# Performance work log

Hardware: AMD Instinct MI355X
Metric: run time of the kernel (lower is better)

The kernel has to match this reference:

```python
import jax, jax.numpy as jnp
import numpy as np

H = 4  # hidden_size
L = 2  # num_layers


def _lstm_cell(x, h, c, Wih, Whh, bih, bhh):
    # PyTorch gate order: input, forget, cell(g), output
    gates = x @ Wih.T + h @ Whh.T + (bih + bhh)  # [B, 4H]
    i, f, g, o = jnp.split(gates, 4, axis=-1)
    i = jax.nn.sigmoid(i)
    f = jax.nn.sigmoid(f)
    g = jnp.tanh(g)
    o = jax.nn.sigmoid(o)
    c_new = f * c + i * g
    h_new = o * jnp.tanh(c_new)
    return h_new, c_new


def setup_inputs() -> dict:
    key = jax.random.key(0)
    ks = jax.random.split(key, 24)
    B, S, D, T = 32768, 256, 8, 12
    s = 1.0 / np.sqrt(H)  # PyTorch LSTM init scale

    def u(k, shape):
        return jax.random.uniform(k, shape, jnp.float32, -s, s)

    inp = {
        "src": jax.random.normal(ks[0], (B, S, D), jnp.float32),
        "trg": jax.random.normal(ks[1], (B, T, 1), jnp.float32),
        # encoder LSTM (input_dim=8 -> H, then H -> H)
        "enc_Wih0": u(ks[2], (4 * H, D)), "enc_Whh0": u(ks[3], (4 * H, H)),
        "enc_bih0": u(ks[4], (4 * H,)), "enc_bhh0": u(ks[5], (4 * H,)),
        "enc_Wih1": u(ks[6], (4 * H, H)), "enc_Whh1": u(ks[7], (4 * H, H)),
        "enc_bih1": u(ks[8], (4 * H,)), "enc_bhh1": u(ks[9], (4 * H,)),
        # decoder LSTM (input_dim=1 -> H, then H -> H)
        "dec_Wih0": u(ks[10], (4 * H, 1)), "dec_Whh0": u(ks[11], (4 * H, H)),
        "dec_bih0": u(ks[12], (4 * H,)), "dec_bhh0": u(ks[13], (4 * H,)),
        "dec_Wih1": u(ks[14], (4 * H, H)), "dec_Whh1": u(ks[15], (4 * H, H)),
        "dec_bih1": u(ks[16], (4 * H,)), "dec_bhh1": u(ks[17], (4 * H,)),
        # fc: hidden -> 1
        "fc_W": u(ks[18], (1, H)), "fc_b": u(ks[19], (1,)),
    }
    return inp


def reference(src, trg,
              enc_Wih0, enc_Whh0, enc_bih0, enc_bhh0,
              enc_Wih1, enc_Whh1, enc_bih1, enc_bhh1,
              dec_Wih0, dec_Whh0, dec_bih0, dec_bhh0,
              dec_Wih1, dec_Whh1, dec_bih1, dec_bhh1,
              fc_W, fc_b):
    B, T = src.shape[0], trg.shape[1]
    enc_layers = [(enc_Wih0, enc_Whh0, enc_bih0, enc_bhh0),
                  (enc_Wih1, enc_Whh1, enc_bih1, enc_bhh1)]
    dec_layers = [(dec_Wih0, dec_Whh0, dec_bih0, dec_bhh0),
                  (dec_Wih1, dec_Whh1, dec_bih1, dec_bhh1)]

    def multi_step(layers, h, c, x):
        new_h, new_c, inp = [], [], x
        for l, p in enumerate(layers):
            hl, cl = _lstm_cell(inp, h[l], c[l], *p)
            new_h.append(hl); new_c.append(cl); inp = hl
        return jnp.stack(new_h), jnp.stack(new_c), inp

    # ---- encoder: scan over src time steps ----
    h0 = jnp.zeros((L, B, H), src.dtype)
    c0 = jnp.zeros((L, B, H), src.dtype)

    def enc_step(carry, x_t):
        h, c = carry
        h, c, _ = multi_step(enc_layers, h, c, x_t)
        return (h, c), None

    (h, c), _ = jax.lax.scan(enc_step, (h0, c0), jnp.swapaxes(src, 0, 1))

    x0 = trg[:, 0, :]  # [B, 1]

    def dec_step(carry, _):
        h, c, x = carry
        h, c, top = multi_step(dec_layers, h, c, x)
        pred = top @ fc_W.T + fc_b  # [B, 1]
        return (h, c, pred), pred

    _, preds = jax.lax.scan(dec_step, (h, c, x0), None, length=T - 1)  # [T-1, B, 1]
    outputs = jnp.concatenate([x0[None], preds], axis=0)  # [T, B, 1]
    return jnp.swapaxes(outputs, 0, 1)  # [B, T, 1]
```

## Files before the change

kernel.cpp:

```cpp
#include <hip/hip_runtime.h>

namespace {

constexpr int Sn = 256;
constexpr int Tn = 12;
constexpr float L2E = 1.44269504088896340736f;

typedef float v2f __attribute__((ext_vector_type(2)));

__device__ __forceinline__ v2f pkfma(v2f a, v2f b, v2f c) {
  return __builtin_elementwise_fma(a, b, c);
}

__device__ __forceinline__ float rcp_(float x) { return __builtin_amdgcn_rcpf(x); }

#if __has_builtin(__builtin_amdgcn_exp2f)
__device__ __forceinline__ float exp2_(float x) { return __builtin_amdgcn_exp2f(x); }
#else
__device__ __forceinline__ float exp2_(float x) { return __expf(x * 0.69314718055994530942f); }
#endif

template <int CTRL>
__device__ __forceinline__ float qperm(float v) {
  return __int_as_float(
      __builtin_amdgcn_mov_dpp(__float_as_int(v), CTRL, 0xF, 0xF, true));
}
constexpr int DPP_XOR1 = 0xB1;
constexpr int DPP_XOR2 = 0x4E;
constexpr int DPP_XOR3 = 0x1B;
constexpr int DPP_BC0 = 0x00;

__device__ __forceinline__ float unit_update(v2f g01, v2f g23, float& c) {
  float ei = exp2_(g01.x);
  float ef = exp2_(g01.y);
  float eg = exp2_(fminf(g23.x, 64.0f));
  float eo = exp2_(g23.y);
  float ig = (eg - 1.0f) * rcp_((1.0f + ei) * (eg + 1.0f));
  float fv = rcp_(1.0f + ef);
  c = fmaf(fv, c, ig);
  float ec = exp2_(fminf(c * (2.0f * L2E), 64.0f));
  return (ec - 1.0f) * rcp_((1.0f + eo) * (ec + 1.0f));
}

__device__ __forceinline__ void quad_gather(float h, float* hg) {
  hg[0] = h;
  hg[1] = qperm<DPP_XOR1>(h);
  hg[2] = qperm<DPP_XOR2>(h);
  hg[3] = qperm<DPP_XOR3>(h);
}

__global__ __launch_bounds__(64) void seq2seq_kernel(
    const float* __restrict__ src, const float* __restrict__ trg,
    const float* __restrict__ eWih0, const float* __restrict__ eWhh0,
    const float* __restrict__ ebih0, const float* __restrict__ ebhh0,
    const float* __restrict__ eWih1, const float* __restrict__ eWhh1,
    const float* __restrict__ ebih1, const float* __restrict__ ebhh1,
    const float* __restrict__ dWih0, const float* __restrict__ dWhh0,
    const float* __restrict__ dbih0, const float* __restrict__ dbhh0,
    const float* __restrict__ dWih1, const float* __restrict__ dWhh1,
    const float* __restrict__ dbih1, const float* __restrict__ dbhh1,
    const float* __restrict__ fcW, const float* __restrict__ fcb,
    float* __restrict__ out) {
  const int gid = blockIdx.x * 64 + threadIdx.x;
  const int e = gid >> 2;
  const int u = gid & 3;

  const int ri = u, rf = 4 + u, rg = 8 + u, ro = 12 + u;

  const v2f s01 = v2f{-L2E, -L2E};
  const v2f s23 = v2f{2.0f * L2E, -L2E};

  v2f w0x01[8], w0x23[8], w0h01[4], w0h23[4];
  v2f w1i01[4], w1i23[4], w1h01[4], w1h23[4];
#pragma unroll
  for (int j = 0; j < 8; ++j) {
    w0x01[j] = v2f{eWih0[ri * 8 + j], eWih0[rf * 8 + j]} * s01;
    w0x23[j] = v2f{eWih0[rg * 8 + j], eWih0[ro * 8 + j]} * s23;
  }
#pragma unroll
  for (int k = 0; k < 4; ++k) {
    const int kc = u ^ k;
    w0h01[k] = v2f{eWhh0[ri * 4 + kc], eWhh0[rf * 4 + kc]} * s01;
    w0h23[k] = v2f{eWhh0[rg * 4 + kc], eWhh0[ro * 4 + kc]} * s23;
    w1i01[k] = v2f{eWih1[ri * 4 + kc], eWih1[rf * 4 + kc]} * s01;
    w1i23[k] = v2f{eWih1[rg * 4 + kc], eWih1[ro * 4 + kc]} * s23;
    w1h01[k] = v2f{eWhh1[ri * 4 + kc], eWhh1[rf * 4 + kc]} * s01;
    w1h23[k] = v2f{eWhh1[rg * 4 + kc], eWhh1[ro * 4 + kc]} * s23;
  }
  const v2f b0_01 = v2f{ebih0[ri] + ebhh0[ri], ebih0[rf] + ebhh0[rf]} * s01;
  const v2f b0_23 = v2f{ebih0[rg] + ebhh0[rg], ebih0[ro] + ebhh0[ro]} * s23;
  const v2f b1_01 = v2f{ebih1[ri] + ebhh1[ri], ebih1[rf] + ebhh1[rf]} * s01;
  const v2f b1_23 = v2f{ebih1[rg] + ebhh1[rg], ebih1[ro] + ebhh1[ro]} * s23;

  const float4* sp = (const float4*)(src + (size_t)e * (Sn * 8));

  float h0g[4] = {0, 0, 0, 0};
  float h1g[4] = {0, 0, 0, 0};
  float c0 = 0.0f, c1 = 0.0f;

  auto enc_step = [&](float4 xa, float4 xb) {
    float x[8] = {xa.x, xa.y, xa.z, xa.w, xb.x, xb.y, xb.z, xb.w};
    v2f a01 = b0_01, a23 = b0_23;
#pragma unroll
    for (int j = 0; j < 8; ++j) {
      v2f xx = v2f{x[j], x[j]};
      a01 = pkfma(xx, w0x01[j], a01);
      a23 = pkfma(xx, w0x23[j], a23);
    }
#pragma unroll
    for (int k = 0; k < 4; ++k) {
      v2f hh = v2f{h0g[k], h0g[k]};
      a01 = pkfma(hh, w0h01[k], a01);
      a23 = pkfma(hh, w0h23[k], a23);
    }
    float h0 = unit_update(a01, a23, c0);
    quad_gather(h0, h0g);

    v2f e01 = b1_01, e23 = b1_23;
#pragma unroll
    for (int k = 0; k < 4; ++k) {
      v2f hh = v2f{h1g[k], h1g[k]};
      e01 = pkfma(hh, w1h01[k], e01);
      e23 = pkfma(hh, w1h23[k], e23);
    }
#pragma unroll
    for (int k = 0; k < 4; ++k) {
      v2f hh = v2f{h0g[k], h0g[k]};
      e01 = pkfma(hh, w1i01[k], e01);
      e23 = pkfma(hh, w1i23[k], e23);
    }
    float h1 = unit_update(e01, e23, c1);
    quad_gather(h1, h1g);
  };

  float4 A[16], B[16];
#pragma unroll
  for (int j = 0; j < 16; ++j) A[j] = sp[j];
#pragma unroll
  for (int j = 0; j < 16; ++j) B[j] = sp[16 + j];

  for (int i = 0; i < 16; ++i) {
#pragma unroll
    for (int s = 0; s < 8; ++s) enc_step(A[2 * s], A[2 * s + 1]);
    if (i < 15) {
#pragma unroll
      for (int j = 0; j < 16; ++j) A[j] = sp[32 * (i + 1) + j];
    }
#pragma unroll
    for (int s = 0; s < 8; ++s) enc_step(B[2 * s], B[2 * s + 1]);
    if (i < 15) {
#pragma unroll
      for (int j = 0; j < 16; ++j) B[j] = sp[32 * (i + 1) + 16 + j];
    }
  }

  v2f dw0i01 = v2f{dWih0[ri], dWih0[rf]} * s01;
  v2f dw0i23 = v2f{dWih0[rg], dWih0[ro]} * s23;
  v2f dw0h01[4], dw0h23[4], dw1i01[4], dw1i23[4], dw1h01[4], dw1h23[4];
#pragma unroll
  for (int k = 0; k < 4; ++k) {
    const int kc = u ^ k;
    dw0h01[k] = v2f{dWhh0[ri * 4 + kc], dWhh0[rf * 4 + kc]} * s01;
    dw0h23[k] = v2f{dWhh0[rg * 4 + kc], dWhh0[ro * 4 + kc]} * s23;
    dw1i01[k] = v2f{dWih1[ri * 4 + kc], dWih1[rf * 4 + kc]} * s01;
    dw1i23[k] = v2f{dWih1[rg * 4 + kc], dWih1[ro * 4 + kc]} * s23;
    dw1h01[k] = v2f{dWhh1[ri * 4 + kc], dWhh1[rf * 4 + kc]} * s01;
    dw1h23[k] = v2f{dWhh1[rg * 4 + kc], dWhh1[ro * 4 + kc]} * s23;
  }
  const v2f db0_01 = v2f{dbih0[ri] + dbhh0[ri], dbih0[rf] + dbhh0[rf]} * s01;
  const v2f db0_23 = v2f{dbih0[rg] + dbhh0[rg], dbih0[ro] + dbhh0[ro]} * s23;
  const v2f db1_01 = v2f{dbih1[ri] + dbhh1[ri], dbih1[rf] + dbhh1[rf]} * s01;
  const v2f db1_23 = v2f{dbih1[rg] + dbhh1[rg], dbih1[ro] + dbhh1[ro]} * s23;
  float fcw[4];
#pragma unroll
  for (int k = 0; k < 4; ++k) fcw[k] = fcW[u ^ k];
  const float fcbv = fcb[0];

  float xv = trg[(size_t)e * Tn];
  if (u == 0) out[(size_t)e * Tn] = xv;

  for (int t = 1; t < Tn; ++t) {
    v2f xx = v2f{xv, xv};
    v2f a01 = pkfma(xx, dw0i01, db0_01);
    v2f a23 = pkfma(xx, dw0i23, db0_23);
#pragma unroll
    for (int k = 0; k < 4; ++k) {
      v2f hh = v2f{h0g[k], h0g[k]};
      a01 = pkfma(hh, dw0h01[k], a01);
      a23 = pkfma(hh, dw0h23[k], a23);
    }
    float h0 = unit_update(a01, a23, c0);
    quad_gather(h0, h0g);

    v2f e01 = db1_01, e23 = db1_23;
#pragma unroll
    for (int k = 0; k < 4; ++k) {
      v2f hh = v2f{h1g[k], h1g[k]};
      e01 = pkfma(hh, dw1h01[k], e01);
      e23 = pkfma(hh, dw1h23[k], e23);
    }
#pragma unroll
    for (int k = 0; k < 4; ++k) {
      v2f hh = v2f{h0g[k], h0g[k]};
      e01 = pkfma(hh, dw1i01[k], e01);
      e23 = pkfma(hh, dw1i23[k], e23);
    }
    float h1 = unit_update(e01, e23, c1);
    quad_gather(h1, h1g);

    float pred = fcbv;
#pragma unroll
    for (int k = 0; k < 4; ++k) pred = fmaf(h1g[k], fcw[k], pred);
    pred = qperm<DPP_BC0>(pred);
    if (u == 0) out[(size_t)e * Tn + t] = pred;
    xv = pred;
  }
}

}

extern "C" void kernel_launch(void* const* d_in, const int* in_sizes, int n_in,
                              void* d_out, int out_size, void* d_ws, size_t ws_size,
                              hipStream_t stream) {
  const float* src = (const float*)d_in[0];
  const float* trg = (const float*)d_in[1];
  const float* eWih0 = (const float*)d_in[2];
  const float* eWhh0 = (const float*)d_in[3];
  const float* ebih0 = (const float*)d_in[4];
  const float* ebhh0 = (const float*)d_in[5];
  const float* eWih1 = (const float*)d_in[6];
  const float* eWhh1 = (const float*)d_in[7];
  const float* ebih1 = (const float*)d_in[8];
  const float* ebhh1 = (const float*)d_in[9];
  const float* dWih0 = (const float*)d_in[10];
  const float* dWhh0 = (const float*)d_in[11];
  const float* dbih0 = (const float*)d_in[12];
  const float* dbhh0 = (const float*)d_in[13];
  const float* dWih1 = (const float*)d_in[14];
  const float* dWhh1 = (const float*)d_in[15];
  const float* dbih1 = (const float*)d_in[16];
  const float* dbhh1 = (const float*)d_in[17];
  const float* fcW = (const float*)d_in[18];
  const float* fcb = (const float*)d_in[19];
  float* out = (float*)d_out;

  const int B = 32768;
  const int lanes = B * 4;
  const int block = 64;
  const int grid = lanes / block;
  seq2seq_kernel<<<grid, block, 0, stream>>>(
      src, trg, eWih0, eWhh0, ebih0, ebhh0, eWih1, eWhh1, ebih1, ebhh1,
      dWih0, dWhh0, dbih0, dbhh0, dWih1, dWhh1, dbih1, dbhh1, fcW, fcb, out);
}
```

Before: 443.4 us.

## Process two batch elements per quad to interleave independent LSTM recurrences

Each 4-lane group now advances two independent batch sequences (e0 and e0+16384) in lockstep, interleaving their FMAs and transcendental updates to hide the serial dependency latency of the recurrence. The grid is halved and the source prefetch buffers shrink to 4 float4 per sequence so register use stays manageable. The cost is fewer waves for latency hiding across the device, with more instruction-level parallelism per wave in exchange.

```diff
diff --git a/kernel.cpp b/kernel.cpp
--- a/kernel.cpp
+++ b/kernel.cpp
@@ -4,6 +4,7 @@
 
 constexpr int Sn = 256;
 constexpr int Tn = 12;
+constexpr int HB = 16384;
 constexpr float L2E = 1.44269504088896340736f;
 
 typedef float v2f __attribute__((ext_vector_type(2)));
@@ -61,9 +62,9 @@
     const float* __restrict__ dbih1, const float* __restrict__ dbhh1,
     const float* __restrict__ fcW, const float* __restrict__ fcb,
     float* __restrict__ out) {
-  const int gid = blockIdx.x * 64 + threadIdx.x;
-  const int e = gid >> 2;
-  const int u = gid & 3;
+  const int slot = blockIdx.x * 64 + threadIdx.x;
+  const int e0 = slot >> 2;
+  const int u = slot & 3;
 
   const int ri = u, rf = 4 + u, rg = 8 + u, ro = 12 + u;
 
@@ -92,65 +93,85 @@
   const v2f b1_01 = v2f{ebih1[ri] + ebhh1[ri], ebih1[rf] + ebhh1[rf]} * s01;
   const v2f b1_23 = v2f{ebih1[rg] + ebhh1[rg], ebih1[ro] + ebhh1[ro]} * s23;
 
-  const float4* sp = (const float4*)(src + (size_t)e * (Sn * 8));
-
-  float h0g[4] = {0, 0, 0, 0};
-  float h1g[4] = {0, 0, 0, 0};
-  float c0 = 0.0f, c1 = 0.0f;
-
-  auto enc_step = [&](float4 xa, float4 xb) {
-    float x[8] = {xa.x, xa.y, xa.z, xa.w, xb.x, xb.y, xb.z, xb.w};
-    v2f a01 = b0_01, a23 = b0_23;
+  const float4* sp0 = (const float4*)(src + (size_t)e0 * (Sn * 8));
+  const float4* sp1 = (const float4*)(src + (size_t)(e0 + HB) * (Sn * 8));
+
+  float h0g[2][4] = {{0, 0, 0, 0}, {0, 0, 0, 0}};
+  float h1g[2][4] = {{0, 0, 0, 0}, {0, 0, 0, 0}};
+  float c0[2] = {0, 0}, c1[2] = {0, 0};
+
+  auto step_pair = [&](float4 xa0, float4 xb0, float4 xa1, float4 xb1) {
+    float x0[8] = {xa0.x, xa0.y, xa0.z, xa0.w, xb0.x, xb0.y, xb0.z, xb0.w};
+    float x1[8] = {xa1.x, xa1.y, xa1.z, xa1.w, xb1.x, xb1.y, xb1.z, xb1.w};
+    v2f a01[2] = {b0_01, b0_01}, a23[2] = {b0_23, b0_23};
 #pragma unroll
     for (int j = 0; j < 8; ++j) {
-      v2f xx = v2f{x[j], x[j]};
-      a01 = pkfma(xx, w0x01[j], a01);
-      a23 = pkfma(xx, w0x23[j], a23);
-    }
-#pragma unroll
-    for (int k = 0; k < 4; ++k) {
-      v2f hh = v2f{h0g[k], h0g[k]};
-      a01 = pkfma(hh, w0h01[k], a01);
-      a23 = pkfma(hh, w0h23[k], a23);
-    }
-    float h0 = unit_update(a01, a23, c0);
-    quad_gather(h0, h0g);
-
-    v2f e01 = b1_01, e23 = b1_23;
-#pragma unroll
-    for (int k = 0; k < 4; ++k) {
-      v2f hh = v2f{h1g[k], h1g[k]};
-      e01 = pkfma(hh, w1h01[k], e01);
-      e23 = pkfma(hh, w1h23[k], e23);
-    }
-#pragma unroll
-    for (int k = 0; k < 4; ++k) {
-      v2f hh = v2f{h0g[k], h0g[k]};
-      e01 = pkfma(hh, w1i01[k], e01);
-      e23 = pkfma(hh, w1i23[k], e23);
-    }
-    float h1 = unit_update(e01, e23, c1);
-    quad_gather(h1, h1g);
+      v2f xx0 = v2f{x0[j], x0[j]};
+      a01[0] = pkfma(xx0, w0x01[j], a01[0]);
+      a23[0] = pkfma(xx0, w0x23[j], a23[0]);
+      v2f xx1 = v2f{x1[j], x1[j]};
+      a01[1] = pkfma(xx1, w0x01[j], a01[1]);
+      a23[1] = pkfma(xx1, w0x23[j], a23[1]);
+    }
+#pragma unroll
+    for (int k = 0; k < 4; ++k) {
+#pragma unroll
+      for (int p = 0; p < 2; ++p) {
+        v2f hh = v2f{h0g[p][k], h0g[p][k]};
+        a01[p] = pkfma(hh, w0h01[k], a01[p]);
+        a23[p] = pkfma(hh, w0h23[k], a23[p]);
+      }
+    }
+    float h0n[2];
+#pragma unroll
+    for (int p = 0; p < 2; ++p) h0n[p] = unit_update(a01[p], a23[p], c0[p]);
+#pragma unroll
+    for (int p = 0; p < 2; ++p) quad_gather(h0n[p], h0g[p]);
+
+    v2f e01[2] = {b1_01, b1_01}, e23[2] = {b1_23, b1_23};
+#pragma unroll
+    for (int k = 0; k < 4; ++k) {
+#pragma unroll
+      for (int p = 0; p < 2; ++p) {
+        v2f hh = v2f{h1g[p][k], h1g[p][k]};
+        e01[p] = pkfma(hh, w1h01[k], e01[p]);
+        e23[p] = pkfma(hh, w1h23[k], e23[p]);
+      }
+    }
+#pragma unroll
+    for (int k = 0; k < 4; ++k) {
+#pragma unroll
+      for (int p = 0; p < 2; ++p) {
+        v2f hh = v2f{h0g[p][k], h0g[p][k]};
+        e01[p] = pkfma(hh, w1i01[k], e01[p]);
+        e23[p] = pkfma(hh, w1i23[k], e23[p]);
+      }
+    }
+    float h1n[2];
+#pragma unroll
+    for (int p = 0; p < 2; ++p) h1n[p] = unit_update(e01[p], e23[p], c1[p]);
+#pragma unroll
+    for (int p = 0; p < 2; ++p) quad_gather(h1n[p], h1g[p]);
   };
 
-  float4 A[16], B[16];
-#pragma unroll
-  for (int j = 0; j < 16; ++j) A[j] = sp[j];
-#pragma unroll
-  for (int j = 0; j < 16; ++j) B[j] = sp[16 + j];
-
-  for (int i = 0; i < 16; ++i) {
-#pragma unroll
-    for (int s = 0; s < 8; ++s) enc_step(A[2 * s], A[2 * s + 1]);
-    if (i < 15) {
-#pragma unroll
-      for (int j = 0; j < 16; ++j) A[j] = sp[32 * (i + 1) + j];
-    }
-#pragma unroll
-    for (int s = 0; s < 8; ++s) enc_step(B[2 * s], B[2 * s + 1]);
-    if (i < 15) {
-#pragma unroll
-      for (int j = 0; j < 16; ++j) B[j] = sp[32 * (i + 1) + 16 + j];
+  float4 A0[4], A1[4], B0[4], B1[4];
+#pragma unroll
+  for (int j = 0; j < 4; ++j) { A0[j] = sp0[j]; A1[j] = sp1[j]; }
+#pragma unroll
+  for (int j = 0; j < 4; ++j) { B0[j] = sp0[4 + j]; B1[j] = sp1[4 + j]; }
+
+  for (int i = 0; i < 64; ++i) {
+    step_pair(A0[0], A0[1], A1[0], A1[1]);
+    step_pair(A0[2], A0[3], A1[2], A1[3]);
+    if (i < 63) {
+#pragma unroll
+      for (int j = 0; j < 4; ++j) { A0[j] = sp0[8 * i + 8 + j]; A1[j] = sp1[8 * i + 8 + j]; }
+    }
+    step_pair(B0[0], B0[1], B1[0], B1[1]);
+    step_pair(B0[2], B0[3], B1[2], B1[3]);
+    if (i < 63) {
+#pragma unroll
+      for (int j = 0; j < 4; ++j) { B0[j] = sp0[8 * i + 12 + j]; B1[j] = sp1[8 * i + 12 + j]; }
     }
   }
 
@@ -176,44 +197,74 @@
   for (int k = 0; k < 4; ++k) fcw[k] = fcW[u ^ k];
   const float fcbv = fcb[0];
 
-  float xv = trg[(size_t)e * Tn];
-  if (u == 0) out[(size_t)e * Tn] = xv;
+  float xv[2] = {trg[(size_t)e0 * Tn], trg[(size_t)(e0 + HB) * Tn]};
+  if (u == 0) {
+    out[(size_t)e0 * Tn] = xv[0];
+    out[(size_t)(e0 + HB) * Tn] = xv[1];
+  }
 
   for (int t = 1; t < Tn; ++t) {
-    v2f xx = v2f{xv, xv};
-    v2f a01 = pkfma(xx, dw0i01, db0_01);
-    v2f a23 = pkfma(xx, dw0i23, db0_23);
-#pragma unroll
-    for (int k = 0; k < 4; ++k) {
-      v2f hh = v2f{h0g[k], h0g[k]};
-      a01 = pkfma(hh, dw0h01[k], a01);
-      a23 = pkfma(hh, dw0h23[k], a23);
-    }
-    float h0 = unit_update(a01, a23, c0);
-    quad_gather(h0, h0g);
-
-    v2f e01 = db1_01, e23 = db1_23;
-#pragma unroll
-    for (int k = 0; k < 4; ++k) {
-      v2f hh = v2f{h1g[k], h1g[k]};
-      e01 = pkfma(hh, dw1h01[k], e01);
-      e23 = pkfma(hh, dw1h23[k], e23);
-    }
-#pragma unroll
-    for (int k = 0; k < 4; ++k) {
-      v2f hh = v2f{h0g[k], h0g[k]};
-      e01 = pkfma(hh, dw1i01[k], e01);
-      e23 = pkfma(hh, dw1i23[k], e23);
-    }
-    float h1 = unit_update(e01, e23, c1);
-    quad_gather(h1, h1g);
-
-    float pred = fcbv;
-#pragma unroll
-    for (int k = 0; k < 4; ++k) pred = fmaf(h1g[k], fcw[k], pred);
-    pred = qperm<DPP_BC0>(pred);
-    if (u == 0) out[(size_t)e * Tn + t] = pred;
-    xv = pred;
+    v2f a01[2], a23[2];
+#pragma unroll
+    for (int p = 0; p < 2; ++p) {
+      v2f xx = v2f{xv[p], xv[p]};
+      a01[p] = pkfma(xx, dw0i01, db0_01);
+      a23[p] = pkfma(xx, dw0i23, db0_23);
+    }
+#pragma unroll
+    for (int k = 0; k < 4; ++k) {
+#pragma unroll
+      for (int p = 0; p < 2; ++p) {
+        v2f hh = v2f{h0g[p][k], h0g[p][k]};
+        a01[p] = pkfma(hh, dw0h01[k], a01[p]);
+        a23[p] = pkfma(hh, dw0h23[k], a23[p]);
+      }
+    }
+    float h0n[2];
+#pragma unroll
+    for (int p = 0; p < 2; ++p) h0n[p] = unit_update(a01[p], a23[p], c0[p]);
+#pragma unroll
+    for (int p = 0; p < 2; ++p) quad_gather(h0n[p], h0g[p]);
+
+    v2f e01[2] = {db1_01, db1_01}, e23[2] = {db1_23, db1_23};
+#pragma unroll
+    for (int k = 0; k < 4; ++k) {
+#pragma unroll
+      for (int p = 0; p < 2; ++p) {
+        v2f hh = v2f{h1g[p][k], h1g[p][k]};
+        e01[p] = pkfma(hh, dw1h01[k], e01[p]);
+        e23[p] = pkfma(hh, dw1h23[k], e23[p]);
+      }
+    }
+#pragma unroll
+    for (int k = 0; k < 4; ++k) {
+#pragma unroll
+      for (int p = 0; p < 2; ++p) {
+        v2f hh = v2f{h0g[p][k], h0g[p][k]};
+        e01[p] = pkfma(hh, dw1i01[k], e01[p]);
+        e23[p] = pkfma(hh, dw1i23[k], e23[p]);
+      }
+    }
+    float h1n[2];
+#pragma unroll
+    for (int p = 0; p < 2; ++p) h1n[p] = unit_update(e01[p], e23[p], c1[p]);
+#pragma unroll
+    for (int p = 0; p < 2; ++p) quad_gather(h1n[p], h1g[p]);
+
+    float pred[2];
+#pragma unroll
+    for (int p = 0; p < 2; ++p) {
+      pred[p] = fcbv;
+#pragma unroll
+      for (int k = 0; k < 4; ++k) pred[p] = fmaf(h1g[p][k], fcw[k], pred[p]);
+      pred[p] = qperm<DPP_BC0>(pred[p]);
+    }
+    if (u == 0) {
+      out[(size_t)e0 * Tn + t] = pred[0];
+      out[(size_t)(e0 + HB) * Tn + t] = pred[1];
+    }
+    xv[0] = pred[0];
+    xv[1] = pred[1];
   }
 }
 
@@ -245,7 +296,7 @@
   float* out = (float*)d_out;
 
   const int B = 32768;
-  const int lanes = B * 4;
+  const int lanes = (B / 2) * 4;
   const int block = 64;
   const int grid = lanes / block;
   seq2seq_kernel<<<grid, block, 0, stream>>>(
```

Measured after the change: 475.9 us. +7.3%, slower.

## Split LSTM layers across lane groups with wavefront-pipelined encoder recurrence

Applied to the files above, without the earlier changes.

Each batch element now gets 8 lanes instead of 4. Layer 0 runs on one quad and layer 1 on the other, and layer 0's hidden state is passed to layer 1 through DPP row shifts. The two layers advance as a skewed pipeline, one tick apart, so each tick's serial dependency chain covers only one layer instead of two, at the cost of doubling lane count and some predicated waste. The encoder no longer batch-prefetches 32 float4 per lane; each lane prefetches just the next step. Launch bounds add an occupancy hint, and the decoder keeps both layers serialized with masked updates.

```diff
diff --git a/kernel.cpp b/kernel.cpp
--- a/kernel.cpp
+++ b/kernel.cpp
@@ -29,6 +29,15 @@
 constexpr int DPP_XOR2 = 0x4E;
 constexpr int DPP_XOR3 = 0x1B;
 constexpr int DPP_BC0 = 0x00;
+
+__device__ __forceinline__ float dpp_shr4_toB(float old, float src) {
+  return __int_as_float(__builtin_amdgcn_update_dpp(
+      __float_as_int(old), __float_as_int(src), 0x114, 0xF, 0xA, false));
+}
+__device__ __forceinline__ float dpp_shl4_toA(float old, float src) {
+  return __int_as_float(__builtin_amdgcn_update_dpp(
+      __float_as_int(old), __float_as_int(src), 0x104, 0xF, 0x5, false));
+}
 
 __device__ __forceinline__ float unit_update(v2f g01, v2f g23, float& c) {
   float ei = exp2_(g01.x);
@@ -49,7 +58,7 @@
   hg[3] = qperm<DPP_XOR3>(h);
 }
 
-__global__ __launch_bounds__(64) void seq2seq_kernel(
+__global__ __launch_bounds__(64, 4) void seq2seq_kernel(
     const float* __restrict__ src, const float* __restrict__ trg,
     const float* __restrict__ eWih0, const float* __restrict__ eWhh0,
     const float* __restrict__ ebih0, const float* __restrict__ ebhh0,
@@ -61,158 +70,171 @@
     const float* __restrict__ dbih1, const float* __restrict__ dbhh1,
     const float* __restrict__ fcW, const float* __restrict__ fcb,
     float* __restrict__ out) {
-  const int gid = blockIdx.x * 64 + threadIdx.x;
-  const int e = gid >> 2;
-  const int u = gid & 3;
+  const int slot = blockIdx.x * 64 + threadIdx.x;
+  const int e = slot >> 3;
+  const int u = slot & 3;
+  const bool grpB = (threadIdx.x & 4) != 0;
 
   const int ri = u, rf = 4 + u, rg = 8 + u, ro = 12 + u;
-
   const v2f s01 = v2f{-L2E, -L2E};
   const v2f s23 = v2f{2.0f * L2E, -L2E};
 
-  v2f w0x01[8], w0x23[8], w0h01[4], w0h23[4];
-  v2f w1i01[4], w1i23[4], w1h01[4], w1h23[4];
+  v2f win01[8], win23[8], wh01[4], wh23[4];
 #pragma unroll
   for (int j = 0; j < 8; ++j) {
-    w0x01[j] = v2f{eWih0[ri * 8 + j], eWih0[rf * 8 + j]} * s01;
-    w0x23[j] = v2f{eWih0[rg * 8 + j], eWih0[ro * 8 + j]} * s23;
-  }
-#pragma unroll
-  for (int k = 0; k < 4; ++k) {
-    const int kc = u ^ k;
-    w0h01[k] = v2f{eWhh0[ri * 4 + kc], eWhh0[rf * 4 + kc]} * s01;
-    w0h23[k] = v2f{eWhh0[rg * 4 + kc], eWhh0[ro * 4 + kc]} * s23;
-    w1i01[k] = v2f{eWih1[ri * 4 + kc], eWih1[rf * 4 + kc]} * s01;
-    w1i23[k] = v2f{eWih1[rg * 4 + kc], eWih1[ro * 4 + kc]} * s23;
-    w1h01[k] = v2f{eWhh1[ri * 4 + kc], eWhh1[rf * 4 + kc]} * s01;
-    w1h23[k] = v2f{eWhh1[rg * 4 + kc], eWhh1[ro * 4 + kc]} * s23;
-  }
-  const v2f b0_01 = v2f{ebih0[ri] + ebhh0[ri], ebih0[rf] + ebhh0[rf]} * s01;
-  const v2f b0_23 = v2f{ebih0[rg] + ebhh0[rg], ebih0[ro] + ebhh0[ro]} * s23;
-  const v2f b1_01 = v2f{ebih1[ri] + ebhh1[ri], ebih1[rf] + ebhh1[rf]} * s01;
-  const v2f b1_23 = v2f{ebih1[rg] + ebhh1[rg], ebih1[ro] + ebhh1[ro]} * s23;
+    v2f vA01 = v2f{eWih0[ri * 8 + j], eWih0[rf * 8 + j]} * s01;
+    v2f vA23 = v2f{eWih0[rg * 8 + j], eWih0[ro * 8 + j]} * s23;
+    if (j < 4) {
+      const int kc = u ^ j;
+      v2f vB01 = v2f{eWih1[ri * 4 + kc], eWih1[rf * 4 + kc]} * s01;
+      v2f vB23 = v2f{eWih1[rg * 4 + kc], eWih1[ro * 4 + kc]} * s23;
+      win01[j] = grpB ? vB01 : vA01;
+      win23[j] = grpB ? vB23 : vA23;
+    } else {
+      win01[j] = grpB ? v2f{0.0f, 0.0f} : vA01;
+      win23[j] = grpB ? v2f{0.0f, 0.0f} : vA23;
+    }
+  }
+  {
+    const float* ph = grpB ? eWhh1 : eWhh0;
+#pragma unroll
+    for (int k = 0; k < 4; ++k) {
+      const int kc = u ^ k;
+      wh01[k] = v2f{ph[ri * 4 + kc], ph[rf * 4 + kc]} * s01;
+      wh23[k] = v2f{ph[rg * 4 + kc], ph[ro * 4 + kc]} * s23;
+    }
+  }
+  const float* pbi = grpB ? ebih1 : ebih0;
+  const float* pbh = grpB ? ebhh1 : ebhh0;
+  const v2f b01 = v2f{pbi[ri] + pbh[ri], pbi[rf] + pbh[rf]} * s01;
+  const v2f b23 = v2f{pbi[rg] + pbh[rg], pbi[ro] + pbh[ro]} * s23;
+  const v2f zb01 = grpB ? v2f{0.0f, 0.0f} : b01;
+  const v2f zb23 = grpB ? v2f{0.0f, 0.0f} : b23;
 
   const float4* sp = (const float4*)(src + (size_t)e * (Sn * 8));
 
-  float h0g[4] = {0, 0, 0, 0};
-  float h1g[4] = {0, 0, 0, 0};
-  float c0 = 0.0f, c1 = 0.0f;
-
-  auto enc_step = [&](float4 xa, float4 xb) {
-    float x[8] = {xa.x, xa.y, xa.z, xa.w, xb.x, xb.y, xb.z, xb.w};
-    v2f a01 = b0_01, a23 = b0_23;
+  float hg[4] = {0, 0, 0, 0};
+  float cv = 0.0f;
+
+  auto tick = [&](float4 xa, float4 xb, v2f bb01, v2f bb23) {
+    float xs[8] = {xa.x, xa.y, xa.z, xa.w, xb.x, xb.y, xb.z, xb.w};
+#pragma unroll
+    for (int j = 0; j < 4; ++j) xs[j] = dpp_shr4_toB(xs[j], hg[j]);
+    v2f a01 = bb01, a23 = bb23;
 #pragma unroll
     for (int j = 0; j < 8; ++j) {
-      v2f xx = v2f{x[j], x[j]};
-      a01 = pkfma(xx, w0x01[j], a01);
-      a23 = pkfma(xx, w0x23[j], a23);
+      v2f xx = v2f{xs[j], xs[j]};
+      a01 = pkfma(xx, win01[j], a01);
+      a23 = pkfma(xx, win23[j], a23);
     }
 #pragma unroll
     for (int k = 0; k < 4; ++k) {
-      v2f hh = v2f{h0g[k], h0g[k]};
-      a01 = pkfma(hh, w0h01[k], a01);
-      a23 = pkfma(hh, w0h23[k], a23);
-    }
-    float h0 = unit_update(a01, a23, c0);
-    quad_gather(h0, h0g);
-
-    v2f e01 = b1_01, e23 = b1_23;
+      v2f hh = v2f{hg[k], hg[k]};
+      a01 = pkfma(hh, wh01[k], a01);
+      a23 = pkfma(hh, wh23[k], a23);
+    }
+    float h = unit_update(a01, a23, cv);
+    quad_gather(h, hg);
+  };
+
+  float4 xa = sp[0], xb = sp[1];
+  float4 na = sp[2], nb = sp[3];
+  tick(xa, xb, zb01, zb23);
+  for (int t = 1; t < Sn; ++t) {
+    float4 ca = na, cb = nb;
+    if (t < Sn - 1) { na = sp[2 * t + 2]; nb = sp[2 * t + 3]; }
+    tick(ca, cb, b01, b23);
+  }
+  {
+    float cs = cv, hs0 = hg[0], hs1 = hg[1], hs2 = hg[2], hs3 = hg[3];
+    tick(na, nb, b01, b23);
+    if (!grpB) { cv = cs; hg[0] = hs0; hg[1] = hs1; hg[2] = hs2; hg[3] = hs3; }
+  }
+
+  v2f dwin01[4], dwin23[4], dwh01[4], dwh23[4];
+#pragma unroll
+  for (int j = 0; j < 4; ++j) {
+    const int kc = u ^ j;
+    v2f vB01 = v2f{dWih1[ri * 4 + kc], dWih1[rf * 4 + kc]} * s01;
+    v2f vB23 = v2f{dWih1[rg * 4 + kc], dWih1[ro * 4 + kc]} * s23;
+    v2f vA01 = (j == 0) ? v2f{dWih0[ri], dWih0[rf]} * s01 : v2f{0.0f, 0.0f};
+    v2f vA23 = (j == 0) ? v2f{dWih0[rg], dWih0[ro]} * s23 : v2f{0.0f, 0.0f};
+    dwin01[j] = grpB ? vB01 : vA01;
+    dwin23[j] = grpB ? vB23 : vA23;
+  }
+  {
+    const float* ph = grpB ? dWhh1 : dWhh0;
 #pragma unroll
     for (int k = 0; k < 4; ++k) {
-      v2f hh = v2f{h1g[k], h1g[k]};
-      e01 = pkfma(hh, w1h01[k], e01);
-      e23 = pkfma(hh, w1h23[k], e23);
-    }
-#pragma unroll
-    for (int k = 0; k < 4; ++k) {
-      v2f hh = v2f{h0g[k], h0g[k]};
-      e01 = pkfma(hh, w1i01[k], e01);
-      e23 = pkfma(hh, w1i23[k], e23);
-    }
-    float h1 = unit_update(e01, e23, c1);
-    quad_gather(h1, h1g);
-  };
-
-  float4 A[16], B[16];
-#pragma unroll
-  for (int j = 0; j < 16; ++j) A[j] = sp[j];
-#pragma unroll
-  for (int j = 0; j < 16; ++j) B[j] = sp[16 + j];
-
-  for (int i = 0; i < 16; ++i) {
-#pragma unroll
-    for (int s = 0; s < 8; ++s) enc_step(A[2 * s], A[2 * s + 1]);
-    if (i < 15) {
-#pragma unroll
-      for (int j = 0; j < 16; ++j) A[j] = sp[32 * (i + 1) + j];
-    }
-#pragma unroll
-    for (int s = 0; s < 8; ++s) enc_step(B[2 * s], B[2 * s + 1]);
-    if (i < 15) {
-#pragma unroll
-      for (int j = 0; j < 16; ++j) B[j] = sp[32 * (i + 1) + 16 + j];
-    }
-  }
-
-  v2f dw0i01 = v2f{dWih0[ri], dWih0[rf]} * s01;
-  v2f dw0i23 = v2f{dWih0[rg], dWih0[ro]} * s23;
-  v2f dw0h01[4], dw0h23[4], dw1i01[4], dw1i23[4], dw1h01[4], dw1h23[4];
-#pragma unroll
-  for (int k = 0; k < 4; ++k) {
-    const int kc = u ^ k;
-    dw0h01[k] = v2f{dWhh0[ri * 4 + kc], dWhh0[rf * 4 + kc]} * s01;
-    dw0h23[k] = v2f{dWhh0[rg * 4 + kc], dWhh0[ro * 4 + kc]} * s23;
-    dw1i01[k] = v2f{dWih1[ri * 4 + kc], dWih1[rf * 4 + kc]} * s01;
-    dw1i23[k] = v2f{dWih1[rg * 4 + kc], dWih1[ro * 4 + kc]} * s23;
-    dw1h01[k] = v2f{dWhh1[ri * 4 + kc], dWhh1[rf * 4 + kc]} * s01;
-    dw1h23[k] = v2f{dWhh1[rg * 4 + kc], dWhh1[ro * 4 + kc]} * s23;
-  }
-  const v2f db0_01 = v2f{dbih0[ri] + dbhh0[ri], dbih0[rf] + dbhh0[rf]} * s01;
-  const v2f db0_23 = v2f{dbih0[rg] + dbhh0[rg], dbih0[ro] + dbhh0[ro]} * s23;
-  const v2f db1_01 = v2f{dbih1[ri] + dbhh1[ri], dbih1[rf] + dbhh1[rf]} * s01;
-  const v2f db1_23 = v2f{dbih1[rg] + dbhh1[rg], dbih1[ro] + dbhh1[ro]} * s23;
+      const int kc = u ^ k;
+      dwh01[k] = v2f{ph[ri * 4 + kc], ph[rf * 4 + kc]} * s01;
+      dwh23[k] = v2f{ph[rg * 4 + kc], ph[ro * 4 + kc]} * s23;
+    }
+  }
+  const float* qbi = grpB ? dbih1 : dbih0;
+  const float* qbh = grpB ? dbhh1 : dbhh0;
+  const v2f db01 = v2f{qbi[ri] + qbh[ri], qbi[rf] + qbh[rf]} * s01;
+  const v2f db23 = v2f{qbi[rg] + qbh[rg], qbi[ro] + qbh[ro]} * s23;
   float fcw[4];
 #pragma unroll
   for (int k = 0; k < 4; ++k) fcw[k] = fcW[u ^ k];
   const float fcbv = fcb[0];
 
   float xv = trg[(size_t)e * Tn];
-  if (u == 0) out[(size_t)e * Tn] = xv;
+  if ((threadIdx.x & 7) == 0) out[(size_t)e * Tn] = xv;
 
   for (int t = 1; t < Tn; ++t) {
-    v2f xx = v2f{xv, xv};
-    v2f a01 = pkfma(xx, dw0i01, db0_01);
-    v2f a23 = pkfma(xx, dw0i23, db0_23);
-#pragma unroll
-    for (int k = 0; k < 4; ++k) {
-      v2f hh = v2f{h0g[k], h0g[k]};
-      a01 = pkfma(hh, dw0h01[k], a01);
-      a23 = pkfma(hh, dw0h23[k], a23);
-    }
-    float h0 = unit_update(a01, a23, c0);
-    quad_gather(h0, h0g);
-
-    v2f e01 = db1_01, e23 = db1_23;
-#pragma unroll
-    for (int k = 0; k < 4; ++k) {
-      v2f hh = v2f{h1g[k], h1g[k]};
-      e01 = pkfma(hh, dw1h01[k], e01);
-      e23 = pkfma(hh, dw1h23[k], e23);
-    }
-#pragma unroll
-    for (int k = 0; k < 4; ++k) {
-      v2f hh = v2f{h0g[k], h0g[k]};
-      e01 = pkfma(hh, dw1i01[k], e01);
-      e23 = pkfma(hh, dw1i23[k], e23);
-    }
-    float h1 = unit_update(e01, e23, c1);
-    quad_gather(h1, h1g);
-
+    {
+      float cT = cv;
+      v2f a01 = db01, a23 = db23;
+      v2f xx = v2f{xv, xv};
+#pragma unroll
+      for (int j = 0; j < 4; ++j) {
+        a01 = pkfma(xx, dwin01[j], a01);
+        a23 = pkfma(xx, dwin23[j], a23);
+      }
+#pragma unroll
+      for (int k = 0; k < 4; ++k) {
+        v2f hh = v2f{hg[k], hg[k]};
+        a01 = pkfma(hh, dwh01[k], a01);
+        a23 = pkfma(hh, dwh23[k], a23);
+      }
+      float hT = unit_update(a01, a23, cT);
+      float hgT[4];
+      quad_gather(hT, hgT);
+      if (!grpB) { cv = cT; hg[0] = hgT[0]; hg[1] = hgT[1]; hg[2] = hgT[2]; hg[3] = hgT[3]; }
+    }
+    {
+      float cT = cv;
+      float xs0 = dpp_shr4_toB(xv, hg[0]);
+      float xs1 = dpp_shr4_toB(xv, hg[1]);
+      float xs2 = dpp_shr4_toB(xv, hg[2]);
+      float xs3 = dpp_shr4_toB(xv, hg[3]);
+      v2f a01 = db01, a23 = db23;
+      float xsv[4] = {xs0, xs1, xs2, xs3};
+#pragma unroll
+      for (int j = 0; j < 4; ++j) {
+        v2f xx = v2f{xsv[j], xsv[j]};
+        a01 = pkfma(xx, dwin01[j], a01);
+        a23 = pkfma(xx, dwin23[j], a23);
+      }
+#pragma unroll
+      for (int k = 0; k < 4; ++k) {
+        v2f hh = v2f{hg[k], hg[k]};
+        a01 = pkfma(hh, dwh01[k], a01);
+        a23 = pkfma(hh, dwh23[k], a23);
+      }
+      float hT = unit_update(a01, a23, cT);
+      float hgT[4];
+      quad_gather(hT, hgT);
+      if (grpB) { cv = cT; hg[0] = hgT[0]; hg[1] = hgT[1]; hg[2] = hgT[2]; hg[3] = hgT[3]; }
+    }
     float pred = fcbv;
 #pragma unroll
-    for (int k = 0; k < 4; ++k) pred = fmaf(h1g[k], fcw[k], pred);
+    for (int k = 0; k < 4; ++k) pred = fmaf(hg[k], fcw[k], pred);
     pred = qperm<DPP_BC0>(pred);
-    if (u == 0) out[(size_t)e * Tn + t] = pred;
+    pred = dpp_shl4_toA(pred, pred);
+    if ((threadIdx.x & 7) == 0) out[(size_t)e * Tn + t] = pred;
     xv = pred;
   }
 }
@@ -245,7 +267,7 @@
   float* out = (float*)d_out;
 
   const int B = 32768;
-  const int lanes = B * 4;
+  const int lanes = B * 8;
   const int block = 64;
   const int grid = lanes / block;
   seq2seq_kernel<<<grid, block, 0, stream>>>(
```

Measured after the change: 470.2 us. 1.06x slower.
